# Kernel optimization log

Hardware: AMD Instinct MI355X
Metric: run time of the kernel (lower is better)

Reference implementation:

```python
import jax, jax.numpy as jnp
import numpy as np

HEADS = 4
BN_EPS = 1e-5


def _linear_attention(x, heads):
    # x: [B, L, C]; per-head linear attention: softmax(Q,dim=feat) @ (softmax(K,dim=seq)^T @ V)
    B, L, C = x.shape
    dh = C // heads
    h = x.reshape(B, L, heads, dh)
    q = jax.nn.softmax(h, axis=-1)          # softmax over feature dim (dim=2 in torch)
    k = jax.nn.softmax(h, axis=1)           # softmax over sequence dim (dim=1 in torch)
    kv = jnp.einsum('blhd,blhe->bhde', k, h)   # [B, H, dh, dh]
    out = jnp.einsum('blhd,bhde->blhe', q, kv) # [B, L, H, dh]
    return out.reshape(B, L, C)


def setup_inputs() -> dict:
    key = jax.random.key(0)
    ks = jax.random.split(key, 10)
    B, C, L, DOUT, NB = 32, 32, 16384, 10, 3
    s = 0.1
    return {
        'x': jax.random.normal(ks[0], (B, C, L), jnp.float32),
        'fcW1': jax.random.normal(ks[1], (NB, C, C), jnp.float32) * s,
        'fcb1': jax.random.normal(ks[2], (NB, C), jnp.float32) * s,
        'fcW2': jax.random.normal(ks[3], (NB, C, C), jnp.float32) * s,
        'fcb2': jax.random.normal(ks[4], (NB, C), jnp.float32) * s,
        'Wh': jax.random.normal(ks[5], (C, C), jnp.float32) * s,
        'bh': jax.random.normal(ks[6], (C,), jnp.float32) * s,
        'bn_gamma': jnp.ones((C,), jnp.float32),
        'bn_beta': jnp.zeros((C,), jnp.float32),
        'bn_mean': jnp.zeros((C,), jnp.float32),
        'bn_var': jnp.ones((C,), jnp.float32),
        'Wf': jax.random.normal(ks[7], (C, DOUT), jnp.float32) * s,
        'bf': jax.random.normal(ks[8], (DOUT,), jnp.float32) * s,
    }


def reference(x, fcW1, fcb1, fcW2, fcb2, Wh, bh, bn_gamma, bn_beta, bn_mean, bn_var, Wf, bf):
    gelu = lambda t: jax.nn.gelu(t, approximate=False)  # torch default GELU is exact erf
    h = jnp.transpose(x, (0, 2, 1))  # [B, C, L] -> [B, L, C]
    n_blocks = fcW1.shape[0]
    for i in range(n_blocks):
        h = _linear_attention(h, HEADS)
        h = gelu(h @ fcW1[i] + fcb1[i])
        h = gelu(h @ fcW2[i] + fcb2[i])
    pooled = jnp.mean(h, axis=1)  # AdaptiveAvgPool1d(1) over L -> [B, C]
    y = pooled @ Wh + bh
    y = (y - bn_mean) * jax.lax.rsqrt(bn_var + BN_EPS) * bn_gamma + bn_beta  # BatchNorm1d (eval)
    y = gelu(y)
    return y @ Wf + bf
```

## Files before the change

### kernel.cpp

```cpp
#include <hip/hip_runtime.h>
#include <cstddef>

#define B_ 32
#define C_ 32
#define L_ 16384
#define H_ 4
#define DH_ 8
#define NB_ 3
#define DOUT_ 10
#define SEG_ 512
#define S_ (L_/SEG_)

#define TILE 256
#define AST  40

typedef _Float16 f16_t;
typedef _Float16 f16x2 __attribute__((ext_vector_type(2)));
typedef _Float16 f16x4 __attribute__((ext_vector_type(4)));
typedef _Float16 f16x8 __attribute__((ext_vector_type(8)));
typedef float    f32x4 __attribute__((ext_vector_type(4)));

__device__ __forceinline__ float gelu_f(float x){
    const float z  = fabsf(x) * 0.70710678118654752440f;
    const float t  = __builtin_amdgcn_rcpf(fmaf(0.47047f, z, 1.0f));
    const float e  = __expf(-z * z);
    float p = fmaf(t, 0.7478556f, -0.0958798f);
    p = fmaf(t, p, 0.3480242f);
    const float erfz = 1.0f - p * t * e;
    const float phi  = fmaf(copysignf(erfz, x), 0.5f, 0.5f);
    return x * phi;
}

#define RED_MAX32(v) do{ v = fmaxf(v, __shfl_xor(v,1));  v = fmaxf(v, __shfl_xor(v,2)); \
                         v = fmaxf(v, __shfl_xor(v,4));  v = fmaxf(v, __shfl_xor(v,8)); \
                         v = fmaxf(v, __shfl_xor(v,16)); }while(0)
#define RED_SUM32(v) do{ v += __shfl_xor(v,1);  v += __shfl_xor(v,2); \
                         v += __shfl_xor(v,4);  v += __shfl_xor(v,8); \
                         v += __shfl_xor(v,16); }while(0)

template<typename T>
__global__ __launch_bounds__(256) void stats_kernel(const T* __restrict__ h,
                                                    float* __restrict__ part,
                                                    float* __restrict__ zpool){
    const int seg = blockIdx.x;
    const int hd  = blockIdx.y;
    const int b   = blockIdx.z;
    const int t   = threadIdx.x;
    const int d   = t >> 5;
    const int j   = t & 31;

    __shared__ float tile[8][SEG_];
    __shared__ float sm[8];

    if (zpool != nullptr && blockIdx.x == 0 && blockIdx.y == 0 && blockIdx.z == 0)
        for (int i = t; i < B_*C_; i += 256) zpool[i] = 0.0f;

    const T* hb = h + (size_t)b * ((size_t)C_*L_) + (size_t)(hd*DH_)*L_ + (size_t)seg*SEG_;

    if constexpr (sizeof(T) == 4){
        for (int f = t; f < 8*SEG_/4; f += 256){
            const int row = f >> 7;
            const int c4  = (f & 127) << 2;
            *(f32x4*)&tile[row][c4] = *(const f32x4*)&hb[(size_t)row*L_ + c4];
        }
    } else {
        for (int f = t; f < 8*SEG_/8; f += 256){
            const int row = f >> 6;
            const int c8  = (f & 63) << 3;
            const f16x8 v = *(const f16x8*)&hb[(size_t)row*L_ + c8];
            f32x4 lo = {(float)v[0], (float)v[1], (float)v[2], (float)v[3]};
            f32x4 hi = {(float)v[4], (float)v[5], (float)v[6], (float)v[7]};
            *(f32x4*)&tile[row][c8]     = lo;
            *(f32x4*)&tile[row][c8 + 4] = hi;
        }
    }
    __syncthreads();

    float m = -INFINITY;
    #pragma unroll
    for (int i = 0; i < SEG_/32; i++) m = fmaxf(m, tile[d][j + 32*i]);
    RED_MAX32(m);
    if (j == 0) sm[d] = m;
    const float m_d = m;

    float s = 0.0f;
    float kv[8];
    #pragma unroll
    for (int e = 0; e < 8; e++) kv[e] = 0.0f;
    #pragma unroll
    for (int i = 0; i < SEG_/32; i++){
        const int k = j + 32*i;
        const float ek = __expf(tile[d][k] - m_d);
        s += ek;
        #pragma unroll
        for (int e = 0; e < 8; e++) kv[e] = fmaf(ek, tile[e][k], kv[e]);
    }
    RED_SUM32(s);
    #pragma unroll
    for (int e = 0; e < 8; e++){ RED_SUM32(kv[e]); }
    __syncthreads();

    float* po = part + (size_t)((b*H_ + hd)*S_ + seg) * 80;
    if (j == 0){
        po[8 + d] = s;
        #pragma unroll
        for (int e = 0; e < 8; e++) po[16 + d*8 + e] = kv[e];
    }
    if (t < 8) po[t] = sm[t];
}

template<bool FIRST, bool LAST>
__global__ __launch_bounds__(256)
__attribute__((amdgpu_waves_per_eu(3, 4)))
void block_kernel(const void* hin,
                  f16_t* hout,
                  const float* __restrict__ part,
                  const float* __restrict__ W1,
                  const float* __restrict__ b1,
                  const float* __restrict__ W2,
                  const float* __restrict__ b2,
                  float* __restrict__ pooled){
    __shared__ __align__(16) f16_t AO[TILE*AST];

    const int tid  = threadIdx.x;
    const int b    = blockIdx.y;
    const int l0   = blockIdx.x * TILE;
    const size_t base = (size_t)b * ((size_t)C_*L_);

    const int wv   = tid >> 6;
    const int lane = tid & 63;
    const int lr   = lane & 15;
    const int lk   = lane >> 4;
    const int posb = l0 + wv*64 + lr;

    float h[4][8];
    if constexpr (FIRST){
        const float* hf = (const float*)hin;
        #pragma unroll
        for (int j = 0; j < 8; j++)
            #pragma unroll
            for (int mt = 0; mt < 4; mt++)
                h[mt][j] = hf[base + (size_t)(lk*8 + j)*L_ + posb + mt*16];
    } else {
        const f16_t* hh = (const f16_t*)hin;
        #pragma unroll
        for (int j = 0; j < 8; j++)
            #pragma unroll
            for (int mt = 0; mt < 4; mt++)
                h[mt][j] = (float)hh[base + (size_t)(lk*8 + j)*L_ + posb + mt*16];
    }

    for (int i = tid; i < 1024; i += 256){
        const int k = i >> 5, n = i & 31;
        AO[(size_t)(128 + n*4 + (k >> 3))*AST + 32 + (k & 7)] = (f16_t)W2[i];
    }
    float bias1[2], bias2[2];
    #pragma unroll
    for (int nt = 0; nt < 2; nt++){ bias1[nt] = b1[nt*16 + lr]; bias2[nt] = b2[nt*16 + lr]; }

    f16x8 a[4];
    #pragma unroll
    for (int mt = 0; mt < 4; mt++){
        float mq = h[mt][0];
        #pragma unroll
        for (int j = 1; j < 8; j++) mq = fmaxf(mq, h[mt][j]);
        float es[8]; float qs = 0.f;
        #pragma unroll
        for (int j = 0; j < 8; j++){ es[j] = __expf(h[mt][j] - mq); qs += es[j]; }
        const float inv = __builtin_amdgcn_rcpf(qs);
        #pragma unroll
        for (int j = 0; j < 8; j++) a[mt][j] = (f16_t)(es[j] * inv);
    }

    const int row = tid >> 3;
    const int qq  = tid & 7;
    const int hdm = row >> 3, dm = row & 7;
    {
        const float* pp = part + (size_t)(b*H_ + hdm) * S_ * 80;
        float pm[4];
        #pragma unroll
        for (int t4 = 0; t4 < 4; t4++) pm[t4] = pp[(qq + 8*t4)*80 + dm];
        float M = fmaxf(fmaxf(pm[0], pm[1]), fmaxf(pm[2], pm[3]));
        float ss = 0.f;
        float kvr[8];
        #pragma unroll
        for (int e = 0; e < 8; e++) kvr[e] = 0.f;
        #pragma unroll
        for (int t4 = 0; t4 < 4; t4++){
            const int s = qq + 8*t4;
            const float sc = __expf(pm[t4] - M);
            ss = fmaf(pp[s*80 + 8 + dm], sc, ss);
            const f32x4 k0 = *(const f32x4*)&pp[s*80 + 16 + dm*8];
            const f32x4 k1 = *(const f32x4*)&pp[s*80 + 16 + dm*8 + 4];
            #pragma unroll
            for (int e = 0; e < 4; e++){
                kvr[e]   = fmaf(k0[e], sc, kvr[e]);
                kvr[4+e] = fmaf(k1[e], sc, kvr[4+e]);
            }
        }
        #pragma unroll
        for (int off = 1; off < 8; off <<= 1){
            const float Mo  = __shfl_xor(M, off);
            const float sso = __shfl_xor(ss, off);
            const float Mn  = fmaxf(M, Mo);
            const float sa  = __expf(M - Mn), sb = __expf(Mo - Mn);
            ss = ss*sa + sso*sb;
            #pragma unroll
            for (int e = 0; e < 8; e++){
                const float ko = __shfl_xor(kvr[e], off);
                kvr[e] = kvr[e]*sa + ko*sb;
            }
            M = Mn;
        }
        const float iss = 1.0f / ss;

        f32x4 acc = {0.f, 0.f, 0.f, 0.f};
        #pragma unroll
        for (int e = 0; e < 8; e++){
            const f32x4 w = *(const f32x4*)&W1[(hdm*8 + e)*32 + qq*4];
            acc += kvr[e] * w;
        }
        #pragma unroll
        for (int j2 = 0; j2 < 4; j2++)
            AO[(size_t)((qq*4 + j2)*4 + hdm)*AST + 32 + dm] = (f16_t)(acc[j2] * iss);
    }
    __syncthreads();

    const f32x4 zero = {0.f, 0.f, 0.f, 0.f};
    f16x8 bw[2];
    f32x4 d[8];

    #pragma unroll
    for (int nt = 0; nt < 2; nt++)
        bw[nt] = *(const f16x8*)&AO[(size_t)((nt*16 + lr)*4 + lk)*AST + 32];
    #pragma unroll
    for (int nt = 0; nt < 2; nt++)
        #pragma unroll
        for (int mt = 0; mt < 4; mt++)
            d[nt*4+mt] = __builtin_amdgcn_mfma_f32_16x16x32_f16(a[mt], bw[nt], zero, 0, 0, 0);

    #pragma unroll
    for (int nt = 0; nt < 2; nt++){
        #pragma unroll
        for (int mt = 0; mt < 4; mt++)
            #pragma unroll
            for (int r = 0; r < 4; r++){
                const float v = gelu_f(d[nt*4+mt][r] + bias1[nt]);
                AO[(size_t)(wv*64 + mt*16 + lk*4 + r)*AST + (nt*16 + lr)] = (f16_t)v;
            }
    }

    f16x8 a2[4];
    #pragma unroll
    for (int mt = 0; mt < 4; mt++)
        a2[mt] = *(const f16x8*)&AO[(size_t)(wv*64 + mt*16 + lr)*AST + lk*8];
    #pragma unroll
    for (int nt = 0; nt < 2; nt++)
        bw[nt] = *(const f16x8*)&AO[(size_t)(128 + (nt*16 + lr)*4 + lk)*AST + 32];
    #pragma unroll
    for (int nt = 0; nt < 2; nt++)
        #pragma unroll
        for (int mt = 0; mt < 4; mt++)
            d[nt*4+mt] = __builtin_amdgcn_mfma_f32_16x16x32_f16(a2[mt], bw[nt], zero, 0, 0, 0);

    #pragma unroll
    for (int nt = 0; nt < 2; nt++)
        #pragma unroll
        for (int mt = 0; mt < 4; mt++)
            #pragma unroll
            for (int r = 0; r < 4; r++)
                d[nt*4+mt][r] = gelu_f(d[nt*4+mt][r] + bias2[nt]);

    if (!LAST){
        #pragma unroll
        for (int nt = 0; nt < 2; nt++)
            #pragma unroll
            for (int mt = 0; mt < 4; mt++){
                const f32x4 dv = d[nt*4+mt];
                f16x4 hv = { (f16_t)dv[0], (f16_t)dv[1], (f16_t)dv[2], (f16_t)dv[3] };
                *(f16x4*)&hout[base + (size_t)(nt*16 + lr)*L_
                               + l0 + wv*64 + mt*16 + lk*4] = hv;
            }
    } else {
        #pragma unroll
        for (int nt = 0; nt < 2; nt++){
            float ps = 0.f;
            #pragma unroll
            for (int mt = 0; mt < 4; mt++)
                ps += d[nt*4+mt][0] + d[nt*4+mt][1] + d[nt*4+mt][2] + d[nt*4+mt][3];
            ps += __shfl_xor(ps, 16);
            ps += __shfl_xor(ps, 32);
            if (lk == 0) atomicAdd(&pooled[b*32 + nt*16 + lr], ps);
        }
    }
}

__global__ __launch_bounds__(1024) void head_kernel(const float* __restrict__ pooled,
                                                    const float* __restrict__ Wh,
                                                    const float* __restrict__ bh,
                                                    const float* __restrict__ gam,
                                                    const float* __restrict__ bet,
                                                    const float* __restrict__ mean,
                                                    const float* __restrict__ var,
                                                    const float* __restrict__ Wf,
                                                    const float* __restrict__ bf,
                                                    float* __restrict__ out){
    __shared__ float y2[32][32];
    const int t = threadIdx.x;
    const int b = t >> 5, c = t & 31;
    float a = bh[c];
    const float invL = 1.0f / (float)L_;
    #pragma unroll
    for (int d = 0; d < 32; d++) a += (pooled[b*32 + d] * invL) * Wh[d*32 + c];
    a = (a - mean[c]) * rsqrtf(var[c] + 1e-5f) * gam[c] + bet[c];
    y2[b][c] = gelu_f(a);
    __syncthreads();
    if (t < B_*DOUT_){
        const int b2 = t / DOUT_, j = t % DOUT_;
        float r = bf[j];
        #pragma unroll
        for (int c2 = 0; c2 < 32; c2++) r += y2[b2][c2] * Wf[c2*DOUT_ + j];
        out[t] = r;
    }
}

extern "C" void kernel_launch(void* const* d_in, const int* in_sizes, int n_in,
                              void* d_out, int out_size, void* d_ws, size_t ws_size,
                              hipStream_t stream){
    (void)in_sizes; (void)n_in; (void)out_size; (void)ws_size;
    const float* x    = (const float*)d_in[0];
    const float* fW1  = (const float*)d_in[1];
    const float* fb1  = (const float*)d_in[2];
    const float* fW2  = (const float*)d_in[3];
    const float* fb2  = (const float*)d_in[4];
    const float* Wh   = (const float*)d_in[5];
    const float* bh   = (const float*)d_in[6];
    const float* gam  = (const float*)d_in[7];
    const float* bet  = (const float*)d_in[8];
    const float* mean = (const float*)d_in[9];
    const float* var  = (const float*)d_in[10];
    const float* Wf   = (const float*)d_in[11];
    const float* bf   = (const float*)d_in[12];
    float* out = (float*)d_out;

    f16_t* hbuf   = (f16_t*)d_ws;
    float* part   = (float*)((char*)d_ws + (size_t)B_*C_*L_*2);
    float* pooled = part + (size_t)B_*H_*S_*80;

    dim3 sgrid(S_, H_, B_);
    dim3 bgrid(L_/TILE, B_);

    stats_kernel<float><<<sgrid, 256, 0, stream>>>(x, part, nullptr);
    block_kernel<true, false><<<bgrid, 256, 0, stream>>>(x, hbuf, part,
        fW1, fb1, fW2, fb2, nullptr);
    stats_kernel<f16_t><<<sgrid, 256, 0, stream>>>(hbuf, part, nullptr);
    block_kernel<false, false><<<bgrid, 256, 0, stream>>>(hbuf, hbuf, part,
        fW1 + C_*C_, fb1 + C_, fW2 + C_*C_, fb2 + C_, nullptr);
    stats_kernel<f16_t><<<sgrid, 256, 0, stream>>>(hbuf, part, pooled);
    block_kernel<false, true><<<bgrid, 256, 0, stream>>>(hbuf, nullptr, part,
        fW1 + 2*C_*C_, fb1 + 2*C_, fW2 + 2*C_*C_, fb2 + 2*C_, pooled);

    head_kernel<<<1, 1024, 0, stream>>>(pooled, Wh, bh, gam, bet, mean, var, Wf, bf, out);
}
```

Measured before the change: 270.1 us.

## Emit fp16 input copy in first stats pass and fuse head into last block

The first stats kernel now also writes an fp16 copy of the input, so the first block kernel reads half-width data instead of fp32. The separate head kernel is removed. The last block to finish, detected with an atomic counter and threadfence, runs the pooled projection, BN, GELU and the final linear layer. This saves one kernel launch and the fp32 reread, but adds an extra fp16 write of the whole input plus an atomic and fence at the end of every block.

```diff
diff --git a/kernel.cpp b/kernel.cpp
--- a/kernel.cpp
+++ b/kernel.cpp
@@ -41,7 +41,8 @@
 template<typename T>
 __global__ __launch_bounds__(256) void stats_kernel(const T* __restrict__ h,
                                                     float* __restrict__ part,
-                                                    float* __restrict__ zpool){
+                                                    float* __restrict__ zpool,
+                                                    f16_t* __restrict__ x16){
     const int seg = blockIdx.x;
     const int hd  = blockIdx.y;
     const int b   = blockIdx.z;
@@ -53,15 +54,22 @@
     __shared__ float sm[8];
 
     if (zpool != nullptr && blockIdx.x == 0 && blockIdx.y == 0 && blockIdx.z == 0)
-        for (int i = t; i < B_*C_; i += 256) zpool[i] = 0.0f;
-
-    const T* hb = h + (size_t)b * ((size_t)C_*L_) + (size_t)(hd*DH_)*L_ + (size_t)seg*SEG_;
+        for (int i = t; i < B_*C_ + 1; i += 256) zpool[i] = 0.0f;
+
+    const size_t boff = (size_t)b * ((size_t)C_*L_) + (size_t)(hd*DH_)*L_ + (size_t)seg*SEG_;
+    const T* hb = h + boff;
 
     if constexpr (sizeof(T) == 4){
+        f16_t* xb = (x16 != nullptr) ? (x16 + boff) : nullptr;
         for (int f = t; f < 8*SEG_/4; f += 256){
             const int row = f >> 7;
             const int c4  = (f & 127) << 2;
-            *(f32x4*)&tile[row][c4] = *(const f32x4*)&hb[(size_t)row*L_ + c4];
+            const f32x4 v = *(const f32x4*)&hb[(size_t)row*L_ + c4];
+            *(f32x4*)&tile[row][c4] = v;
+            if (xb != nullptr){
+                f16x4 hv = { (f16_t)v[0], (f16_t)v[1], (f16_t)v[2], (f16_t)v[3] };
+                *(f16x4*)&xb[(size_t)row*L_ + c4] = hv;
+            }
         }
     } else {
         for (int f = t; f < 8*SEG_/8; f += 256){
@@ -109,17 +117,27 @@
     if (t < 8) po[t] = sm[t];
 }
 
-template<bool FIRST, bool LAST>
+template<bool LAST>
 __global__ __launch_bounds__(256)
 __attribute__((amdgpu_waves_per_eu(3, 4)))
-void block_kernel(const void* hin,
+void block_kernel(const f16_t* hin,
                   f16_t* hout,
                   const float* __restrict__ part,
                   const float* __restrict__ W1,
                   const float* __restrict__ b1,
                   const float* __restrict__ W2,
                   const float* __restrict__ b2,
-                  float* __restrict__ pooled){
+                  float* pooled,
+                  unsigned* done,
+                  const float* __restrict__ Whp,
+                  const float* __restrict__ bhp,
+                  const float* __restrict__ gamp,
+                  const float* __restrict__ betp,
+                  const float* __restrict__ meanp,
+                  const float* __restrict__ varp,
+                  const float* __restrict__ Wfp,
+                  const float* __restrict__ bfp,
+                  float* __restrict__ outp){
     __shared__ __align__(16) f16_t AO[TILE*AST];
 
     const int tid  = threadIdx.x;
@@ -134,21 +152,11 @@
     const int posb = l0 + wv*64 + lr;
 
     float h[4][8];
-    if constexpr (FIRST){
-        const float* hf = (const float*)hin;
-        #pragma unroll
-        for (int j = 0; j < 8; j++)
-            #pragma unroll
-            for (int mt = 0; mt < 4; mt++)
-                h[mt][j] = hf[base + (size_t)(lk*8 + j)*L_ + posb + mt*16];
-    } else {
-        const f16_t* hh = (const f16_t*)hin;
-        #pragma unroll
-        for (int j = 0; j < 8; j++)
-            #pragma unroll
-            for (int mt = 0; mt < 4; mt++)
-                h[mt][j] = (float)hh[base + (size_t)(lk*8 + j)*L_ + posb + mt*16];
-    }
+    #pragma unroll
+    for (int j = 0; j < 8; j++)
+        #pragma unroll
+        for (int mt = 0; mt < 4; mt++)
+            h[mt][j] = (float)hin[base + (size_t)(lk*8 + j)*L_ + posb + mt*16];
 
     for (int i = tid; i < 1024; i += 256){
         const int k = i >> 5, n = i & 31;
@@ -292,35 +300,36 @@
             ps += __shfl_xor(ps, 32);
             if (lk == 0) atomicAdd(&pooled[b*32 + nt*16 + lr], ps);
         }
-    }
-}
-
-__global__ __launch_bounds__(1024) void head_kernel(const float* __restrict__ pooled,
-                                                    const float* __restrict__ Wh,
-                                                    const float* __restrict__ bh,
-                                                    const float* __restrict__ gam,
-                                                    const float* __restrict__ bet,
-                                                    const float* __restrict__ mean,
-                                                    const float* __restrict__ var,
-                                                    const float* __restrict__ Wf,
-                                                    const float* __restrict__ bf,
-                                                    float* __restrict__ out){
-    __shared__ float y2[32][32];
-    const int t = threadIdx.x;
-    const int b = t >> 5, c = t & 31;
-    float a = bh[c];
-    const float invL = 1.0f / (float)L_;
-    #pragma unroll
-    for (int d = 0; d < 32; d++) a += (pooled[b*32 + d] * invL) * Wh[d*32 + c];
-    a = (a - mean[c]) * rsqrtf(var[c] + 1e-5f) * gam[c] + bet[c];
-    y2[b][c] = gelu_f(a);
-    __syncthreads();
-    if (t < B_*DOUT_){
-        const int b2 = t / DOUT_, j = t % DOUT_;
-        float r = bf[j];
-        #pragma unroll
-        for (int c2 = 0; c2 < 32; c2++) r += y2[b2][c2] * Wf[c2*DOUT_ + j];
-        out[t] = r;
+        __threadfence();
+        volatile unsigned* lastfp = (volatile unsigned*)&AO[TILE*AST - 2];
+        __syncthreads();
+        if (tid == 0){
+            const unsigned old = atomicAdd(done, 1u);
+            *lastfp = (old == (unsigned)((L_/TILE)*B_ - 1)) ? 1u : 0u;
+        }
+        __syncthreads();
+        if (*lastfp){
+            __threadfence();
+            float* y2 = (float*)AO;
+            const float invL = 1.0f / (float)L_;
+            for (int i = tid; i < B_*C_; i += 256){
+                const int bb = i >> 5, cc = i & 31;
+                float acc = bhp[cc];
+                #pragma unroll
+                for (int d2 = 0; d2 < 32; d2++)
+                    acc += (pooled[bb*32 + d2] * invL) * Whp[d2*32 + cc];
+                acc = (acc - meanp[cc]) * rsqrtf(varp[cc] + 1e-5f) * gamp[cc] + betp[cc];
+                y2[i] = gelu_f(acc);
+            }
+            __syncthreads();
+            for (int i = tid; i < B_*DOUT_; i += 256){
+                const int b2 = i / DOUT_, jj = i % DOUT_;
+                float r = bfp[jj];
+                #pragma unroll
+                for (int c2 = 0; c2 < 32; c2++) r += y2[b2*32 + c2] * Wfp[c2*DOUT_ + jj];
+                outp[i] = r;
+            }
+        }
     }
 }
 
@@ -346,19 +355,21 @@
     f16_t* hbuf   = (f16_t*)d_ws;
     float* part   = (float*)((char*)d_ws + (size_t)B_*C_*L_*2);
     float* pooled = part + (size_t)B_*H_*S_*80;
+    unsigned* done = (unsigned*)(pooled + B_*C_);
 
     dim3 sgrid(S_, H_, B_);
     dim3 bgrid(L_/TILE, B_);
 
-    stats_kernel<float><<<sgrid, 256, 0, stream>>>(x, part, nullptr);
-    block_kernel<true, false><<<bgrid, 256, 0, stream>>>(x, hbuf, part,
-        fW1, fb1, fW2, fb2, nullptr);
-    stats_kernel<f16_t><<<sgrid, 256, 0, stream>>>(hbuf, part, nullptr);
-    block_kernel<false, false><<<bgrid, 256, 0, stream>>>(hbuf, hbuf, part,
-        fW1 + C_*C_, fb1 + C_, fW2 + C_*C_, fb2 + C_, nullptr);
-    stats_kernel<f16_t><<<sgrid, 256, 0, stream>>>(hbuf, part, pooled);
-    block_kernel<false, true><<<bgrid, 256, 0, stream>>>(hbuf, nullptr, part,
-        fW1 + 2*C_*C_, fb1 + 2*C_, fW2 + 2*C_*C_, fb2 + 2*C_, pooled);
-
-    head_kernel<<<1, 1024, 0, stream>>>(pooled, Wh, bh, gam, bet, mean, var, Wf, bf, out);
+    stats_kernel<float><<<sgrid, 256, 0, stream>>>(x, part, nullptr, hbuf);
+    block_kernel<false><<<bgrid, 256, 0, stream>>>(hbuf, hbuf, part,
+        fW1, fb1, fW2, fb2, nullptr, nullptr,
+        nullptr, nullptr, nullptr, nullptr, nullptr, nullptr, nullptr, nullptr, nullptr);
+    stats_kernel<f16_t><<<sgrid, 256, 0, stream>>>(hbuf, part, nullptr, nullptr);
+    block_kernel<false><<<bgrid, 256, 0, stream>>>(hbuf, hbuf, part,
+        fW1 + C_*C_, fb1 + C_, fW2 + C_*C_, fb2 + C_, nullptr, nullptr,
+        nullptr, nullptr, nullptr, nullptr, nullptr, nullptr, nullptr, nullptr, nullptr);
+    stats_kernel<f16_t><<<sgrid, 256, 0, stream>>>(hbuf, part, pooled, nullptr);
+    block_kernel<true><<<bgrid, 256, 0, stream>>>(hbuf, nullptr, part,
+        fW1 + 2*C_*C_, fb1 + 2*C_, fW2 + 2*C_*C_, fb2 + 2*C_, pooled, done,
+        Wh, bh, gam, bet, mean, var, Wf, bf, out);
 }
```

After: 389.0 us. +44.0%, slower.
